# Performance work log

Hardware: AMD Instinct MI355X
Metric: run time of the kernel (lower is better)

Reference implementation:

```python
import jax, jax.numpy as jnp
import numpy as np

N, IN_DIM, OUT_DIM = 8192, 256, 128
NEG_BIG = -9e15


def setup_inputs() -> dict:
    key = jax.random.key(0)
    k_x, k_a, k_w, k_att = jax.random.split(key, 4)
    X = jax.random.normal(k_x, (N, IN_DIM), dtype=jnp.float32)
    A = jax.random.randint(k_a, (N, N), 0, 2).astype(jnp.float32)
    # nn.Linear(in_dim, out_dim, bias=False): weight [out_dim, in_dim]
    W = jax.random.normal(k_w, (OUT_DIM, IN_DIM), dtype=jnp.float32) / np.sqrt(IN_DIM)
    # nn.Linear(out_dim, 1, bias=False): weight [1, out_dim] -> store as [out_dim]
    a_w = jax.random.normal(k_att, (OUT_DIM,), dtype=jnp.float32) / np.sqrt(OUT_DIM)
    return {"X": X, "A": A, "W": W, "a_w": a_w}


def reference(X, A, W, a_w):
    Wh = X @ W.T                                  # [N, out_dim]
    e = jax.nn.relu(Wh) @ a_w                      # [N]  (a(relu(Wh)).squeeze(-1))
    # NOTE: faithful to source: e broadcasts over rows -> score[i, j] = e[j]
    scores = jnp.where(A > 0, e[None, :], NEG_BIG)  # [N, N]
    attention = jax.nn.softmax(scores, axis=1)      # [N, N]
    h_prime = attention @ Wh                        # [N, out_dim]
    return jax.nn.relu(h_prime)
```

## Files before the change

### kernel.cpp

```cpp
#include <hip/hip_runtime.h>

typedef float        f32x4  __attribute__((ext_vector_type(4)));
typedef __bf16       bf16x8 __attribute__((ext_vector_type(8)));
typedef __bf16       bf16x4 __attribute__((ext_vector_type(4)));
typedef unsigned int u32x4  __attribute__((ext_vector_type(4)));

#define NN   8192
#define IND  256
#define OUTD 128
#define KCHUNK 128
#define ASTR 136
#define BSTR 136

__device__ __forceinline__ bf16x8 cvt2(f32x4 a, f32x4 b) {
  bf16x8 r;
  r[0]=(__bf16)a[0]; r[1]=(__bf16)a[1]; r[2]=(__bf16)a[2]; r[3]=(__bf16)a[3];
  r[4]=(__bf16)b[0]; r[5]=(__bf16)b[1]; r[6]=(__bf16)b[2]; r[7]=(__bf16)b[3];
  return r;
}

__global__ __launch_bounds__(256) void k1_bt(const float* __restrict__ X,
                                             const float* __restrict__ W,
                                             const float* __restrict__ aw,
                                             __bf16* __restrict__ Bt) {
  __shared__ float red[4][16][128];
  const int tid  = threadIdx.x;
  const int lane = tid & 63;
  const int wave = tid >> 6;
  const int nlo  = lane & 15;
  const int quad = lane >> 4;
  const int rowBase = blockIdx.x * 16;

  const float* xp = X + (size_t)(rowBase + nlo) * IND + wave * 64 + quad * 8;
  f32x4 acc[8];
#pragma unroll
  for (int nt = 0; nt < 8; ++nt) acc[nt] = f32x4{0.f, 0.f, 0.f, 0.f};

#pragma unroll
  for (int kb = 0; kb < 64; kb += 32) {
    f32x4 a0 = *(const f32x4*)(xp + kb);
    f32x4 a1 = *(const f32x4*)(xp + kb + 4);
    bf16x8 af = cvt2(a0, a1);
#pragma unroll
    for (int nt = 0; nt < 8; ++nt) {
      const float* wp = W + (size_t)(nt * 16 + nlo) * IND + wave * 64 + kb + quad * 8;
      f32x4 b0 = *(const f32x4*)wp;
      f32x4 b1 = *(const f32x4*)(wp + 4);
      acc[nt] = __builtin_amdgcn_mfma_f32_16x16x32_bf16(af, cvt2(b0, b1), acc[nt], 0, 0, 0);
    }
  }
#pragma unroll
  for (int nt = 0; nt < 8; ++nt)
#pragma unroll
    for (int rg = 0; rg < 4; ++rg)
      red[wave][quad * 4 + rg][nt * 16 + nlo] = acc[nt][rg];
  __syncthreads();

  const int r  = tid >> 4;
  const int c0 = (tid & 15) * 8;
  f32x4 vlo = *(const f32x4*)&red[0][r][c0];
  f32x4 vhi = *(const f32x4*)&red[0][r][c0 + 4];
#pragma unroll
  for (int w = 1; w < 4; ++w) {
    vlo += *(const f32x4*)&red[w][r][c0];
    vhi += *(const f32x4*)&red[w][r][c0 + 4];
  }
  float pa = 0.f;
#pragma unroll
  for (int i = 0; i < 4; ++i) {
    pa += fmaxf(vlo[i], 0.f) * aw[c0 + i];
    pa += fmaxf(vhi[i], 0.f) * aw[c0 + 4 + i];
  }
#pragma unroll
  for (int off = 8; off; off >>= 1) pa += __shfl_xor(pa, off, 64);
  const float wexp = expf(pa);
  const int j = rowBase + r;

#pragma unroll
  for (int i = 0; i < 4; ++i)
    Bt[(size_t)(c0 + i) * NN + j] = (__bf16)(vlo[i] * wexp);
#pragma unroll
  for (int i = 0; i < 4; ++i)
    Bt[(size_t)(c0 + 4 + i) * NN + j] = (__bf16)(vhi[i] * wexp);
  if ((tid & 15) == 0)
    Bt[(size_t)OUTD * NN + j] = (__bf16)wexp;
  if (tid < 120) {
    const int row = 129 + (tid >> 3);
    const int cc  = rowBase + (tid & 7) * 2;
    Bt[(size_t)row * NN + cc]     = (__bf16)0.f;
    Bt[(size_t)row * NN + cc + 1] = (__bf16)0.f;
  }
}

__global__ __launch_bounds__(256) void k3_fused(const float* __restrict__ Adj,
                                                const __bf16* __restrict__ Bt,
                                                float* __restrict__ out) {
  __shared__ unsigned short aT[32 * ASTR];
  __shared__ unsigned short bT[144 * BSTR];
  __shared__ float dend[32];
  const int tid  = threadIdx.x;
  const int lane = tid & 63;
  const int wv   = tid >> 6;
  const int nlo  = lane & 15;
  const int quad = lane >> 4;
  const int rowgrp = wv & 1;
  const int ntgrp  = wv >> 1;
  const int nt0 = ntgrp ? 5 : 0;
  const int ntn = ntgrp ? 4 : 5;
  const int rowBase = blockIdx.x * 32;

  const int arow = tid >> 3;
  const int acol = (tid & 7) * 16;
  const int brow = tid >> 4;
  const int bcol = (tid & 15) * 8;

  const float*  aload = Adj + (size_t)(rowBase + arow) * NN + acol;
  const __bf16* bload = Bt + (size_t)brow * NN + bcol;

  f32x4 acc[5];
#pragma unroll
  for (int t = 0; t < 5; ++t) acc[t] = f32x4{0.f, 0.f, 0.f, 0.f};

  for (int c = 0; c < NN / KCHUNK; ++c) {
    const int kc = c * KCHUNK;
    u32x4 breg[9];
#pragma unroll
    for (int rr = 0; rr < 9; ++rr)
      breg[rr] = *(const u32x4*)(bload + (size_t)(rr * 16) * NN + kc);
    f32x4 areg[4];
#pragma unroll
    for (int j = 0; j < 4; ++j)
      areg[j] = __builtin_nontemporal_load((const f32x4*)(aload + kc + j * 4));
#pragma unroll
    for (int rr = 0; rr < 9; ++rr)
      *(u32x4*)(bT + (rr * 16 + brow) * BSTR + bcol) = breg[rr];
    *(bf16x8*)(aT + arow * ASTR + acol)     = cvt2(areg[0], areg[1]);
    *(bf16x8*)(aT + arow * ASTR + acol + 8) = cvt2(areg[2], areg[3]);
    __syncthreads();

#pragma unroll
    for (int s = 0; s < 4; ++s) {
      bf16x8 af = *(const bf16x8*)(aT + (rowgrp * 16 + nlo) * ASTR + s * 32 + quad * 8);
#pragma unroll
      for (int t = 0; t < 5; ++t) {
        if (t < ntn) {
          bf16x8 bf = *(const bf16x8*)(bT + ((nt0 + t) * 16 + nlo) * BSTR + s * 32 + quad * 8);
          acc[t] = __builtin_amdgcn_mfma_f32_16x16x32_bf16(af, bf, acc[t], 0, 0, 0);
        }
      }
    }
    __syncthreads();
  }

  if (ntgrp == 1 && nlo == 0) {
#pragma unroll
    for (int rg = 0; rg < 4; ++rg)
      dend[rowgrp * 16 + quad * 4 + rg] = acc[3][rg];
  }
  __syncthreads();

  const int nstore = ntgrp ? 3 : 5;
#pragma unroll
  for (int rg = 0; rg < 4; ++rg) {
    const float den = dend[rowgrp * 16 + quad * 4 + rg];
    const int row = rowBase + rowgrp * 16 + quad * 4 + rg;
#pragma unroll
    for (int t = 0; t < 5; ++t) {
      if (t < nstore)
        out[(size_t)row * OUTD + (nt0 + t) * 16 + nlo] = fmaxf(acc[t][rg] / den, 0.f);
    }
  }
}

extern "C" void kernel_launch(void* const* d_in, const int* in_sizes, int n_in,
                              void* d_out, int out_size, void* d_ws, size_t ws_size,
                              hipStream_t stream) {
  const float* X  = (const float*)d_in[0];
  const float* A  = (const float*)d_in[1];
  const float* W  = (const float*)d_in[2];
  const float* aw = (const float*)d_in[3];
  float* out = (float*)d_out;

  __bf16* Bt = (__bf16*)d_ws;

  k1_bt<<<512, 256, 0, stream>>>(X, W, aw, Bt);
  k3_fused<<<256, 256, 0, stream>>>(A, Bt, out);
}
```

Before: 448.0 us.

## Halve rows per block in fused attention kernel to double grid size

The fused attention-matmul kernel now handles 16 adjacency rows per block instead of 32 and launches 512 blocks instead of 256. Work is redistributed so each wave owns two 16-column output tiles, and wave 0 also computes the denominator tile. A launch-bounds occupancy hint of 3 blocks per SM is added. The goal is to fill more CUs on a 256-CU part and raise memory-level parallelism for streaming the fp32 adjacency matrix, at the cost of reloading the shared Bt tile twice as often overall and putting uneven MFMA work on wave 0.

```diff
diff --git a/kernel.cpp b/kernel.cpp
--- a/kernel.cpp
+++ b/kernel.cpp
@@ -2,7 +2,6 @@
 
 typedef float        f32x4  __attribute__((ext_vector_type(4)));
 typedef __bf16       bf16x8 __attribute__((ext_vector_type(8)));
-typedef __bf16       bf16x4 __attribute__((ext_vector_type(4)));
 typedef unsigned int u32x4  __attribute__((ext_vector_type(4)));
 
 #define NN   8192
@@ -92,34 +91,26 @@
   }
 }
 
-__global__ __launch_bounds__(256) void k3_fused(const float* __restrict__ Adj,
-                                                const __bf16* __restrict__ Bt,
-                                                float* __restrict__ out) {
-  __shared__ unsigned short aT[32 * ASTR];
+__global__ __launch_bounds__(256, 3) void k3_fused(const float* __restrict__ Adj,
+                                                   const __bf16* __restrict__ Bt,
+                                                   float* __restrict__ out) {
+  __shared__ unsigned short aT[16 * ASTR];
   __shared__ unsigned short bT[144 * BSTR];
-  __shared__ float dend[32];
+  __shared__ float dend[16];
   const int tid  = threadIdx.x;
   const int lane = tid & 63;
   const int wv   = tid >> 6;
   const int nlo  = lane & 15;
   const int quad = lane >> 4;
-  const int rowgrp = wv & 1;
-  const int ntgrp  = wv >> 1;
-  const int nt0 = ntgrp ? 5 : 0;
-  const int ntn = ntgrp ? 4 : 5;
-  const int rowBase = blockIdx.x * 32;
+  const int rowBase = blockIdx.x * 16;
 
-  const int arow = tid >> 3;
-  const int acol = (tid & 7) * 16;
-  const int brow = tid >> 4;
-  const int bcol = (tid & 15) * 8;
+  const int srow = tid >> 4;
+  const int scol = (tid & 15) * 8;
 
-  const float*  aload = Adj + (size_t)(rowBase + arow) * NN + acol;
-  const __bf16* bload = Bt + (size_t)brow * NN + bcol;
+  const float*  aload = Adj + (size_t)(rowBase + srow) * NN + scol;
+  const __bf16* bload = Bt + (size_t)srow * NN + scol;
 
-  f32x4 acc[5];
-#pragma unroll
-  for (int t = 0; t < 5; ++t) acc[t] = f32x4{0.f, 0.f, 0.f, 0.f};
+  f32x4 acc0 = {0.f,0.f,0.f,0.f}, acc1 = {0.f,0.f,0.f,0.f}, acc2 = {0.f,0.f,0.f,0.f};
 
   for (int c = 0; c < NN / KCHUNK; ++c) {
     const int kc = c * KCHUNK;
@@ -127,48 +118,41 @@
 #pragma unroll
     for (int rr = 0; rr < 9; ++rr)
       breg[rr] = *(const u32x4*)(bload + (size_t)(rr * 16) * NN + kc);
-    f32x4 areg[4];
-#pragma unroll
-    for (int j = 0; j < 4; ++j)
-      areg[j] = __builtin_nontemporal_load((const f32x4*)(aload + kc + j * 4));
+    f32x4 a0 = __builtin_nontemporal_load((const f32x4*)(aload + kc));
+    f32x4 a1 = __builtin_nontemporal_load((const f32x4*)(aload + kc + 4));
 #pragma unroll
     for (int rr = 0; rr < 9; ++rr)
-      *(u32x4*)(bT + (rr * 16 + brow) * BSTR + bcol) = breg[rr];
-    *(bf16x8*)(aT + arow * ASTR + acol)     = cvt2(areg[0], areg[1]);
-    *(bf16x8*)(aT + arow * ASTR + acol + 8) = cvt2(areg[2], areg[3]);
+      *(u32x4*)(bT + (rr * 16 + srow) * BSTR + scol) = breg[rr];
+    *(bf16x8*)(aT + srow * ASTR + scol) = cvt2(a0, a1);
     __syncthreads();
 
 #pragma unroll
     for (int s = 0; s < 4; ++s) {
-      bf16x8 af = *(const bf16x8*)(aT + (rowgrp * 16 + nlo) * ASTR + s * 32 + quad * 8);
-#pragma unroll
-      for (int t = 0; t < 5; ++t) {
-        if (t < ntn) {
-          bf16x8 bf = *(const bf16x8*)(bT + ((nt0 + t) * 16 + nlo) * BSTR + s * 32 + quad * 8);
-          acc[t] = __builtin_amdgcn_mfma_f32_16x16x32_bf16(af, bf, acc[t], 0, 0, 0);
-        }
+      bf16x8 af = *(const bf16x8*)(aT + nlo * ASTR + s * 32 + quad * 8);
+      bf16x8 b0 = *(const bf16x8*)(bT + (wv * 16 + nlo) * BSTR + s * 32 + quad * 8);
+      acc0 = __builtin_amdgcn_mfma_f32_16x16x32_bf16(af, b0, acc0, 0, 0, 0);
+      bf16x8 b1 = *(const bf16x8*)(bT + ((wv + 4) * 16 + nlo) * BSTR + s * 32 + quad * 8);
+      acc1 = __builtin_amdgcn_mfma_f32_16x16x32_bf16(af, b1, acc1, 0, 0, 0);
+      if (wv == 0) {
+        bf16x8 b2 = *(const bf16x8*)(bT + (128 + nlo) * BSTR + s * 32 + quad * 8);
+        acc2 = __builtin_amdgcn_mfma_f32_16x16x32_bf16(af, b2, acc2, 0, 0, 0);
       }
     }
     __syncthreads();
   }
 
-  if (ntgrp == 1 && nlo == 0) {
+  if (wv == 0 && nlo == 0) {
 #pragma unroll
-    for (int rg = 0; rg < 4; ++rg)
-      dend[rowgrp * 16 + quad * 4 + rg] = acc[3][rg];
+    for (int rg = 0; rg < 4; ++rg) dend[quad * 4 + rg] = acc2[rg];
   }
   __syncthreads();
 
-  const int nstore = ntgrp ? 3 : 5;
 #pragma unroll
   for (int rg = 0; rg < 4; ++rg) {
-    const float den = dend[rowgrp * 16 + quad * 4 + rg];
-    const int row = rowBase + rowgrp * 16 + quad * 4 + rg;
-#pragma unroll
-    for (int t = 0; t < 5; ++t) {
-      if (t < nstore)
-        out[(size_t)row * OUTD + (nt0 + t) * 16 + nlo] = fmaxf(acc[t][rg] / den, 0.f);
-    }
+    const int row = quad * 4 + rg;
+    const float den = dend[row];
+    out[(size_t)(rowBase + row) * OUTD + wv * 16 + nlo]       = fmaxf(acc0[rg] / den, 0.f);
+    out[(size_t)(rowBase + row) * OUTD + (wv + 4) * 16 + nlo] = fmaxf(acc1[rg] / den, 0.f);
   }
 }
 
@@ -184,5 +168,5 @@
   __bf16* Bt = (__bf16*)d_ws;
 
   k1_bt<<<512, 256, 0, stream>>>(X, W, aw, Bt);
-  k3_fused<<<256, 256, 0, stream>>>(A, Bt, out);
+  k3_fused<<<512, 256, 0, stream>>>(A, Bt, out);
 }
```

Result: faster. 438.1 us (-2.2%).
